# Kernel tuning notes

Hardware: AMD Instinct MI355X
Metric: run time of the kernel (lower is better)

Reference implementation:

```python
import jax, jax.numpy as jnp
import numpy as np
from jax import lax

HS, WS = 8, 8  # pattern_size


def setup_inputs() -> dict:
    key = jax.random.key(0)
    k1, k2, k3 = jax.random.split(key, 3)
    B, C, T, H, W = 2, 64, 16, 112, 112
    Cout, K = 64, 3
    x = jax.random.normal(k1, (B, C, T, H, W), dtype=jnp.float32)
    # one independent Conv3d weight/bias per (h, w) phase in the 8x8 pattern
    weight = jax.random.normal(k2, (HS, WS, Cout, C, K, K, K), dtype=jnp.float32) * 0.05
    bias = jax.random.normal(k3, (HS, WS, Cout), dtype=jnp.float32) * 0.05
    return {"x": x, "weight": weight, "bias": bias}


def reference(x, weight, bias):
    hs, ws = HS, WS
    B, C, T, H, W = x.shape
    Cout = weight.shape[2]
    # torch F.pad(x, (hs-1, hs-1, ws-1, ws-1, 1, 1)): W padded by hs-1, H by ws-1, T by 1
    paded = jnp.pad(x, ((0, 0), (0, 0), (1, 1), (ws - 1, ws - 1), (hs - 1, hs - 1)))
    Ho, Wo = H // hs, W // ws  # conv output spatial size per phase: (H-3)//8 + 1 = H//8
    rows = []
    for h in range(hs):
        cols = []
        for w in range(ws):
            sl = paded[:, :, :, h:H + h, w:W + w]  # [B, C, T+2, H, W]
            y = lax.conv_general_dilated(
                sl, weight[h, w],
                window_strides=(1, hs, ws), padding='VALID',
                dimension_numbers=('NCDHW', 'OIDHW', 'NCDHW'))  # [B, Cout, T, Ho, Wo]
            cols.append(y + bias[h, w][None, :, None, None, None])
        rows.append(jnp.stack(cols, 0))
    res = jnp.stack(rows, 0)  # [hs, ws, B, Cout, T, Ho, Wo]
    # out[:, :, :, h + hs*i, w + ws*j] = res[h, w, :, :, :, i, j]
    out = jnp.transpose(res, (2, 3, 4, 5, 0, 6, 1))  # [B, Cout, T, Ho, hs, Wo, ws]
    return out.reshape(B, Cout, T, H, W)
```

## Files before the change

kernel.cpp:

```cpp
#include <hip/hip_runtime.h>
#include <hip/hip_bf16.h>
#include <stdint.h>

typedef __attribute__((ext_vector_type(8))) short short8;
typedef __attribute__((ext_vector_type(4))) float f32x4;

#define XPP_BYTES 66355200ull
#define XPP_SLACK 65536ull
#define WPP_BYTES 14155776ull

__device__ __forceinline__ void gl2lds16(const void* g, void* l) {
    __builtin_amdgcn_global_load_lds(
        (const __attribute__((address_space(1))) unsigned int*)g,
        (__attribute__((address_space(3))) unsigned int*)l, 16, 0, 0);
}

__global__ __launch_bounds__(256)
void bzero(uint4* __restrict__ xpp) {
    const uint4 z = {0u, 0u, 0u, 0u};
    const int total = 935936;
    for (int idx = blockIdx.x * 256 + threadIdx.x; idx < total;
         idx += gridDim.x * 256) {
        int u;
        if (idx < 276480) {
            int slab = idx / 2160, off = idx % 2160;
            u = slab * 32400 + off;
        } else if (idx < 534528) {
            int k = idx - 276480;
            int run = k / 144, off = k % 144;
            int slab = run / 14, rho = run % 14 + 1;
            u = slab * 32400 + rho * 2160 + off;
        } else {
            int k = idx - 534528;
            int run = k / 8, off = k % 8;
            int slab = run / 392, r2 = run % 392;
            int rho = r2 / 28 + 1, r3 = r2 % 28;
            int cwo = r3 / 2 + 1, d = (r3 & 1) * 17;
            u = slab * 32400 + rho * 2160 + cwo * 144 + d * 8 + off;
        }
        xpp[u] = z;
    }
}

__global__ __launch_bounds__(512)
void xform_x(const float* __restrict__ xin, __hip_bfloat16* __restrict__ xpp) {
    extern __shared__ __hip_bfloat16 Xl[];
    const int bid = blockIdx.x;
    const int rho = bid % 14, d = (bid / 14) % 16, b = bid / 224;
    const int tid = threadIdx.x;
    for (int f = tid; f < 64 * 8 * 28; f += 512) {
        int ci = f / 224, rem = f % 224;
        int r = rem / 28, c4 = (rem % 28) * 4;
        const float4 v = *(const float4*)&xin[
            ((((size_t)b * 64 + ci) * 16 + d) * 112 + (rho * 8 + r)) * 112 + c4];
        const float vv[4] = {v.x, v.y, v.z, v.w};
#pragma unroll
        for (int u = 0; u < 4; ++u) {
            int c = c4 + u;
            Xl[(r * 112 + c) * 64 + (ci ^ ((c & 7) << 3))] = __float2bfloat16(vv[u]);
        }
    }
    __syncthreads();
    for (int f = tid; f < 896 * 8; f += 512) {
        int pos = f >> 3, j = f & 7;
        int r = pos / 112, c = pos % 112;
        int cw = c & 7, cwo = c >> 3;
        uint4 v = *(const uint4*)&Xl[pos * 64 + ((j * 8) ^ ((c & 7) << 3))];
        size_t dst = (((((size_t)(r * 8 + cw) * 2 + b) * 15 + (rho + 1)) * 15
                       + (cwo + 1)) * 18 + (d + 1)) * 64 + j * 8;
        *(uint4*)(xpp + dst) = v;
    }
}

__global__ __launch_bounds__(256)
void xform_w(const float* __restrict__ wt, __hip_bfloat16* __restrict__ wpp) {
    __shared__ __hip_bfloat16 lw[8 * 27 * 72];
    const int hw = blockIdx.x >> 3, cc = blockIdx.x & 7;
    for (int f = threadIdx.x; f < 8 * 64 * 27; f += 256) {
        int k = f % 27, ci = (f / 27) % 64, co = f / (27 * 64);
        float v = wt[(size_t)hw * 110592 + (size_t)(cc * 8 + co) * 1728 + ci * 27 + k];
        lw[(co * 27 + k) * 72 + ci] = __float2bfloat16(v);
    }
    __syncthreads();
    for (int f = threadIdx.x; f < 27 * 8 * 8; f += 256) {
        int cic = f % 8, co = (f / 8) % 8, k = f / 64;
        uint4 v = *(const uint4*)&lw[(co * 27 + k) * 72 + cic * 8];
        size_t dst = (((size_t)hw * 27 + k) * 64 + (cc * 8 + co)) * 64 + cic * 8;
        *(uint4*)(wpp + dst) = v;
    }
}


#define STG(S) do {                                                          \
    const int s3_ = (S);                                                     \
    const int rr_ = s3_ >> 1, kh_ = rr_ / 3, kw_ = rr_ % 3;                  \
    const int r0_ = h + kh_ - 7, c0_ = w + kw_ - 7;                          \
    const char* ap_ = (const char*)xpp +                                     \
        (size_t)(((((r0_ & 7) * 8 + (c0_ & 7)) * 2 + b) * 15                 \
                  + ((r0_ >> 3) + 1 + mc)) * 15 + ((c0_ >> 3) + 1)) * 2304   \
        + (s3_ & 1) * 64;                                                    \
    char* Ad_ = smem + (s3_ & 3) * 16384;                                    \
    _Pragma("unroll")                                                        \
    for (int i_ = 0; i_ < 4; ++i_)                                           \
        gl2lds16(ap_ + srcoff[i_], Ad_ + (uint32_t)(tid + i_ * 256) * 16);   \
} while (0)

#define LDB(R, DST) do {                                                     \
    const char* bp_ = wbase + (size_t)(R) * 8192;                            \
    _Pragma("unroll")                                                        \
    for (int kd_ = 0; kd_ < 3; ++kd_)                                        \
    _Pragma("unroll")                                                        \
    for (int ks_ = 0; ks_ < 2; ++ks_)                                        \
    _Pragma("unroll")                                                        \
    for (int n_ = 0; n_ < 2; ++n_)                                           \
        DST[kd_ * 4 + ks_ * 2 + n_] = *(const short8*)(                      \
            bp_ + kd_ * 73728 + (ng * 2 + n_) * 2048 + ks_ * 64 + bofs);     \
} while (0)

#define WINDOW(S, R, CUR, NXT, KS, DOB, DOA, WAITN) do {                     \
    if ((WAITN) == 0)      asm volatile("s_waitcnt vmcnt(0)" ::: "memory");  \
    else if ((WAITN) == 4) asm volatile("s_waitcnt vmcnt(4)" ::: "memory");  \
    else if ((WAITN) == 8) asm volatile("s_waitcnt vmcnt(8)" ::: "memory");  \
    else                   asm volatile("s_waitcnt vmcnt(20)" ::: "memory"); \
    __builtin_amdgcn_s_barrier();                                            \
    {   const char* Ab_ = smem + ((S) & 3) * 16384;                          \
        _Pragma("unroll")                                                    \
        for (int kd = 0; kd < 3; ++kd) {                                     \
            short8 af_[7];                                                   \
            _Pragma("unroll")                                                \
            for (int j_ = 0; j_ < 7; ++j_)                                   \
                af_[j_] = *(const short8*)(Ab_ + (mg * 7 + j_) * 1152        \
                                           + rofs[kd]);                      \
            if (kd == 0) {                                                   \
                __builtin_amdgcn_sched_barrier(0);                           \
                if (DOB) LDB((R) + 1, NXT);                                  \
                if (DOA) STG((S) + 3);                                       \
                __builtin_amdgcn_sched_barrier(0);                           \
            }                                                                \
            __builtin_amdgcn_s_setprio(1);                                   \
            _Pragma("unroll")                                                \
            for (int j_ = 0; j_ < 7; ++j_)                                   \
                _Pragma("unroll")                                            \
                for (int n_ = 0; n_ < 2; ++n_)                               \
                    acc[j_][n_] = __builtin_amdgcn_mfma_f32_16x16x32_bf16(   \
                        af_[j_], CUR[kd * 4 + (KS) * 2 + n_],                \
                        acc[j_][n_], 0, 0, 0);                               \
            __builtin_amdgcn_s_setprio(0);                                   \
        } }                                                                  \
} while (0)

__global__ __launch_bounds__(256, 2)
void patgemm(const __hip_bfloat16* __restrict__ xpp,
             const __hip_bfloat16* __restrict__ wpp,
             const float* __restrict__ bs,
             float* __restrict__ out) {
    extern __shared__ char smem[];
    const int bid = blockIdx.x;
    const int h = bid & 7, k = bid >> 3;
    const int w = k & 7, b = (k >> 3) & 1, mc = k >> 4;
    const int hw = h * 8 + w;
    const int tid = threadIdx.x, wv = tid >> 6, lane = tid & 63;
    const int col = lane & 15, quad = lane >> 4;
    const int mg = wv >> 1, ng = wv & 1;

    uint32_t srcoff[4];
#pragma unroll
    for (int i = 0; i < 4; ++i) {
        int u = tid + i * 256; if (u > 1007) u = 1007;
        int wo = u / 72, rem = u % 72;
        int d = rem >> 2, qp = rem & 3, q = qp ^ ((d >> 1) & 3);
        srcoff[i] = (uint32_t)(wo * 2304 + d * 128 + q * 16);
    }
    uint32_t rofs[3];
#pragma unroll
    for (int kd = 0; kd < 3; ++kd)
        rofs[kd] = (uint32_t)((col + kd) * 64
            + ((quad ^ (((col + kd) >> 1) & 3)) << 4));
    const uint32_t bofs = (uint32_t)(col * 128 + quad * 16);

    f32x4 acc[7][2];
#pragma unroll
    for (int j = 0; j < 7; ++j)
#pragma unroll
        for (int n = 0; n < 2; ++n) acc[j][n] = (f32x4){0.f, 0.f, 0.f, 0.f};

    const char* wbase = (const char*)wpp + (size_t)hw * 27 * 8192;
    short8 bfrA[12], bfrB[12];

    STG(0);
    __builtin_amdgcn_sched_barrier(0);
    LDB(0, bfrA);
    __builtin_amdgcn_sched_barrier(0);
    STG(1);
    STG(2);

#pragma unroll 1
    for (int rp = 0; rp < 4; ++rp) {
        const int ra = 2 * rp, rb = 2 * rp + 1;
        WINDOW(2 * ra,     ra, bfrA, bfrB, 0, 1, 1, 8);
        WINDOW(2 * ra + 1, ra, bfrA, bfrB, 1, 0, 1, 20);
        WINDOW(2 * rb,     rb, bfrB, bfrA, 0, 1, 1, 8);
        WINDOW(2 * rb + 1, rb, bfrB, bfrA, 1, 0, (rb < 7), 20);
    }
    WINDOW(16, 8, bfrA, bfrB, 0, 0, 0, 4);
    WINDOW(17, 8, bfrA, bfrB, 1, 0, 0, 0);

    const float* bsl = bs + hw * 64;
    const int y = 8 * mc + h;
#pragma unroll
    for (int j = 0; j < 7; ++j) {
        const int wo = mg * 7 + j;
        const int x = 8 * wo + w;
#pragma unroll
        for (int n = 0; n < 2; ++n) {
            const int co = (ng * 2 + n) * 16 + col;
            const float bv = bsl[co];
#pragma unroll
            for (int jj = 0; jj < 4; ++jj) {
                const int t = quad * 4 + jj;
                out[((((size_t)b * 64 + co) * 16 + t) * 112 + y) * 112 + x]
                    = acc[j][n][jj] + bv;
            }
        }
    }
}

#define XL_ROWSTRIDE 116
#define WL_WSTRIDE (17*27)

__global__ __launch_bounds__(256, 3)
void patconv3d_fp32(const float* __restrict__ xin,
                    const float* __restrict__ wt,
                    const float* __restrict__ bs,
                    float* __restrict__ out) {
    __shared__ float Xl[3*3*7*XL_ROWSTRIDE];
    __shared__ float Wl[8*WL_WSTRIDE];
    const int bid = blockIdx.x;
    const int ct = bid & 3, hb = (bid >> 2) & 1, h = (bid >> 3) & 7;
    const int t = (bid >> 6) & 15, b = (bid >> 10) & 1;
    const int tid = threadIdx.x;
    const int xl = tid & 127, cg = tid >> 7;
    const int xr = (xl < 112) ? xl : 111;
    const int wq = xl & 7;
    float acc[8][7];
#pragma unroll
    for (int c = 0; c < 8; ++c)
#pragma unroll
        for (int ho = 0; ho < 7; ++ho) acc[c][ho] = 0.f;
    for (int ci = 0; ci < 64; ++ci) {
        __syncthreads();
        for (int idx = tid; idx < 3 * 3 * 7 * 114; idx += 256) {
            int c = idx % 114, rest = idx / 114;
            int ho = rest % 7; rest /= 7;
            int kh = rest % 3, kd = rest / 3;
            int r = 8 * (hb * 7 + ho) + h + kh - 7;
            int d = t + kd - 1, colx = c - 7;
            float v = 0.f;
            if (r >= 0 && d >= 0 && d < 16 && colx >= 0)
                v = xin[(((size_t)(b * 64 + ci) * 16 + d) * 112 + r) * 112 + colx];
            Xl[((kd * 3 + kh) * 7 + ho) * XL_ROWSTRIDE + c] = v;
        }
        for (int idx = tid; idx < 8 * 16 * 27; idx += 256) {
            int k2 = idx % 27, rest = idx / 27;
            int co_l = rest % 16, wi = rest / 16;
            Wl[wi * WL_WSTRIDE + co_l * 27 + k2] =
                wt[(((size_t)(h * 8 + wi) * 64 + (ct * 16 + co_l)) * 64 + ci) * 27 + k2];
        }
        __syncthreads();
#pragma unroll
        for (int kd = 0; kd < 3; ++kd)
#pragma unroll
            for (int kh = 0; kh < 3; ++kh)
#pragma unroll
                for (int kw = 0; kw < 3; ++kw) {
                    const int k2 = (kd * 3 + kh) * 3 + kw;
                    float xv[7];
#pragma unroll
                    for (int ho = 0; ho < 7; ++ho)
                        xv[ho] = Xl[((kd * 3 + kh) * 7 + ho) * XL_ROWSTRIDE + xr + kw];
                    float wv[8];
#pragma unroll
                    for (int c = 0; c < 8; ++c)
                        wv[c] = Wl[wq * WL_WSTRIDE + (cg * 8 + c) * 27 + k2];
#pragma unroll
                    for (int c = 0; c < 8; ++c)
#pragma unroll
                        for (int ho = 0; ho < 7; ++ho)
                            acc[c][ho] += wv[c] * xv[ho];
                }
    }
    if (xl < 112) {
#pragma unroll
        for (int c = 0; c < 8; ++c) {
            const int co = ct * 16 + cg * 8 + c;
            const float bv = bs[(h * 8 + wq) * 64 + co];
#pragma unroll
            for (int ho = 0; ho < 7; ++ho) {
                const int y = 8 * (hb * 7 + ho) + h;
                out[(((size_t)(b * 64 + co) * 16 + t) * 112 + y) * 112 + xl] = acc[c][ho] + bv;
            }
        }
    }
}

extern "C" void kernel_launch(void* const* d_in, const int* in_sizes, int n_in,
                              void* d_out, int out_size, void* d_ws, size_t ws_size,
                              hipStream_t stream) {
    const float* x  = (const float*)d_in[0];
    const float* wg = (const float*)d_in[1];
    const float* bi = (const float*)d_in[2];
    float* out = (float*)d_out;
    if (ws_size >= XPP_BYTES + XPP_SLACK + WPP_BYTES) {
        __hip_bfloat16* xpp = (__hip_bfloat16*)d_ws;
        __hip_bfloat16* wpp = (__hip_bfloat16*)((char*)d_ws + XPP_BYTES + XPP_SLACK);
        bzero<<<1024, 256, 0, stream>>>((uint4*)d_ws);
        xform_x<<<448, 512, 114688, stream>>>(x, xpp);
        xform_w<<<512, 256, 0, stream>>>(wg, wpp);
        patgemm<<<1792, 256, 65536, stream>>>(xpp, wpp, bi, out);
    } else {
        patconv3d_fp32<<<2048, 256, 0, stream>>>(x, wg, bi, out);
    }
}
```

Before: 303.0 us.

## Double patgemm waves per block, splitting N across four waves

The patgemm block grows from 256 to 512 threads. Each wave now owns one 16-wide slice of output channels instead of two, which halves the per-wave B fragments and accumulators. Weight fragments are prefetched one K-step (stage) ahead instead of one filter row ahead, and the wait counts and LDS staging loads are rebalanced across the larger block. The aim is to cut register pressure, raise occupancy and latency hiding, and shorten each wave's serial MFMA chain. The cost is that each A fragment read from LDS is reused by fewer MFMAs, so LDS traffic per FLOP roughly doubles, and each stage needs more barriers.

```diff
diff --git a/kernel.cpp b/kernel.cpp
--- a/kernel.cpp
+++ b/kernel.cpp
@@ -101,27 +101,22 @@
         + (s3_ & 1) * 64;                                                    \
     char* Ad_ = smem + (s3_ & 3) * 16384;                                    \
     _Pragma("unroll")                                                        \
-    for (int i_ = 0; i_ < 4; ++i_)                                           \
-        gl2lds16(ap_ + srcoff[i_], Ad_ + (uint32_t)(tid + i_ * 256) * 16);   \
+    for (int i_ = 0; i_ < 2; ++i_)                                           \
+        gl2lds16(ap_ + srcoff[i_], Ad_ + (uint32_t)(tid + i_ * 512) * 16);   \
 } while (0)
 
-#define LDB(R, DST) do {                                                     \
-    const char* bp_ = wbase + (size_t)(R) * 8192;                            \
+#define LDB(S, DST) do {                                                     \
+    const int sb_ = (S);                                                     \
+    const char* bp_ = wbase + (size_t)(sb_ >> 1) * 8192 + (sb_ & 1) * 64;    \
     _Pragma("unroll")                                                        \
     for (int kd_ = 0; kd_ < 3; ++kd_)                                        \
-    _Pragma("unroll")                                                        \
-    for (int ks_ = 0; ks_ < 2; ++ks_)                                        \
-    _Pragma("unroll")                                                        \
-    for (int n_ = 0; n_ < 2; ++n_)                                           \
-        DST[kd_ * 4 + ks_ * 2 + n_] = *(const short8*)(                      \
-            bp_ + kd_ * 73728 + (ng * 2 + n_) * 2048 + ks_ * 64 + bofs);     \
+        DST[kd_] = *(const short8*)(bp_ + kd_ * 73728 + ng * 2048 + bofs);   \
 } while (0)
 
-#define WINDOW(S, R, CUR, NXT, KS, DOB, DOA, WAITN) do {                     \
+#define WINDOW(S, CUR, NXT, DOB, DOA, WAITN) do {                            \
     if ((WAITN) == 0)      asm volatile("s_waitcnt vmcnt(0)" ::: "memory");  \
     else if ((WAITN) == 4) asm volatile("s_waitcnt vmcnt(4)" ::: "memory");  \
-    else if ((WAITN) == 8) asm volatile("s_waitcnt vmcnt(8)" ::: "memory");  \
-    else                   asm volatile("s_waitcnt vmcnt(20)" ::: "memory"); \
+    else                   asm volatile("s_waitcnt vmcnt(2)" ::: "memory");  \
     __builtin_amdgcn_s_barrier();                                            \
     {   const char* Ab_ = smem + ((S) & 3) * 16384;                          \
         _Pragma("unroll")                                                    \
@@ -133,23 +128,21 @@
                                            + rofs[kd]);                      \
             if (kd == 0) {                                                   \
                 __builtin_amdgcn_sched_barrier(0);                           \
-                if (DOB) LDB((R) + 1, NXT);                                  \
+                if (DOB) LDB((S) + 1, NXT);                                  \
+                __builtin_amdgcn_sched_barrier(0);                           \
                 if (DOA) STG((S) + 3);                                       \
                 __builtin_amdgcn_sched_barrier(0);                           \
             }                                                                \
             __builtin_amdgcn_s_setprio(1);                                   \
             _Pragma("unroll")                                                \
             for (int j_ = 0; j_ < 7; ++j_)                                   \
-                _Pragma("unroll")                                            \
-                for (int n_ = 0; n_ < 2; ++n_)                               \
-                    acc[j_][n_] = __builtin_amdgcn_mfma_f32_16x16x32_bf16(   \
-                        af_[j_], CUR[kd * 4 + (KS) * 2 + n_],                \
-                        acc[j_][n_], 0, 0, 0);                               \
+                acc[j_] = __builtin_amdgcn_mfma_f32_16x16x32_bf16(           \
+                    af_[j_], CUR[kd], acc[j_], 0, 0, 0);                     \
             __builtin_amdgcn_s_setprio(0);                                   \
         } }                                                                  \
 } while (0)
 
-__global__ __launch_bounds__(256, 2)
+__global__ __launch_bounds__(512, 4)
 void patgemm(const __hip_bfloat16* __restrict__ xpp,
              const __hip_bfloat16* __restrict__ wpp,
              const float* __restrict__ bs,
@@ -161,12 +154,12 @@
     const int hw = h * 8 + w;
     const int tid = threadIdx.x, wv = tid >> 6, lane = tid & 63;
     const int col = lane & 15, quad = lane >> 4;
-    const int mg = wv >> 1, ng = wv & 1;
-
-    uint32_t srcoff[4];
-#pragma unroll
-    for (int i = 0; i < 4; ++i) {
-        int u = tid + i * 256; if (u > 1007) u = 1007;
+    const int mg = wv >> 2, ng = wv & 3;
+
+    uint32_t srcoff[2];
+#pragma unroll
+    for (int i = 0; i < 2; ++i) {
+        int u = tid + i * 512; if (u > 1007) u = 1007;
         int wo = u / 72, rem = u % 72;
         int d = rem >> 2, qp = rem & 3, q = qp ^ ((d >> 1) & 3);
         srcoff[i] = (uint32_t)(wo * 2304 + d * 128 + q * 16);
@@ -178,14 +171,12 @@
             + ((quad ^ (((col + kd) >> 1) & 3)) << 4));
     const uint32_t bofs = (uint32_t)(col * 128 + quad * 16);
 
-    f32x4 acc[7][2];
-#pragma unroll
-    for (int j = 0; j < 7; ++j)
-#pragma unroll
-        for (int n = 0; n < 2; ++n) acc[j][n] = (f32x4){0.f, 0.f, 0.f, 0.f};
+    f32x4 acc[7];
+#pragma unroll
+    for (int j = 0; j < 7; ++j) acc[j] = (f32x4){0.f, 0.f, 0.f, 0.f};
 
     const char* wbase = (const char*)wpp + (size_t)hw * 27 * 8192;
-    short8 bfrA[12], bfrB[12];
+    short8 bfrA[3], bfrB[3];
 
     STG(0);
     __builtin_amdgcn_sched_barrier(0);
@@ -194,33 +185,30 @@
     STG(1);
     STG(2);
 
+    WINDOW(0, bfrA, bfrB, 1, 1, 4);
 #pragma unroll 1
-    for (int rp = 0; rp < 4; ++rp) {
-        const int ra = 2 * rp, rb = 2 * rp + 1;
-        WINDOW(2 * ra,     ra, bfrA, bfrB, 0, 1, 1, 8);
-        WINDOW(2 * ra + 1, ra, bfrA, bfrB, 1, 0, 1, 20);
-        WINDOW(2 * rb,     rb, bfrB, bfrA, 0, 1, 1, 8);
-        WINDOW(2 * rb + 1, rb, bfrB, bfrA, 1, 0, (rb < 7), 20);
-    }
-    WINDOW(16, 8, bfrA, bfrB, 0, 0, 0, 4);
-    WINDOW(17, 8, bfrA, bfrB, 1, 0, 0, 0);
+    for (int kp = 0; kp < 7; ++kp) {
+        const int s1 = 2 * kp + 1;
+        WINDOW(s1,     bfrB, bfrA, 1, 1, 2);
+        WINDOW(s1 + 1, bfrA, bfrB, 1, 1, 2);
+    }
+    WINDOW(15, bfrB, bfrA, 1, 0, 2);
+    WINDOW(16, bfrA, bfrB, 1, 0, 0);
+    WINDOW(17, bfrB, bfrA, 0, 0, 0);
 
     const float* bsl = bs + hw * 64;
     const int y = 8 * mc + h;
+    const int co = ng * 16 + col;
+    const float bv = bsl[co];
 #pragma unroll
     for (int j = 0; j < 7; ++j) {
         const int wo = mg * 7 + j;
         const int x = 8 * wo + w;
 #pragma unroll
-        for (int n = 0; n < 2; ++n) {
-            const int co = (ng * 2 + n) * 16 + col;
-            const float bv = bsl[co];
-#pragma unroll
-            for (int jj = 0; jj < 4; ++jj) {
-                const int t = quad * 4 + jj;
-                out[((((size_t)b * 64 + co) * 16 + t) * 112 + y) * 112 + x]
-                    = acc[j][n][jj] + bv;
-            }
+        for (int jj = 0; jj < 4; ++jj) {
+            const int t = quad * 4 + jj;
+            out[((((size_t)b * 64 + co) * 16 + t) * 112 + y) * 112 + x]
+                = acc[j][jj] + bv;
         }
     }
 }
@@ -316,7 +304,7 @@
         bzero<<<1024, 256, 0, stream>>>((uint4*)d_ws);
         xform_x<<<448, 512, 114688, stream>>>(x, xpp);
         xform_w<<<512, 256, 0, stream>>>(wg, wpp);
-        patgemm<<<1792, 256, 65536, stream>>>(xpp, wpp, bi, out);
+        patgemm<<<1792, 512, 65536, stream>>>(xpp, wpp, bi, out);
     } else {
         patconv3d_fp32<<<2048, 256, 0, stream>>>(x, wg, bi, out);
     }
```

Measured after the change: 298.0 us. Within noise of the previous version (-1.6%).

## Switch patgemm to 32x32x16 MFMA with 7-wave blocks covering two output rows

Applied to the files above, without the earlier changes.

Rewrites the main GEMM kernel to use 32x32x16 bf16 MFMA tiles instead of 16x16x32. Each 448-thread block now covers two output rows (mcp) with 7 waves, which halves the grid. The weight layout is repacked so each lane loads its B fragment with a contiguous 16-byte read. The A-tile staging moves to a 3-stage ring of larger LDS buffers, and the K loop is fully unrolled with per-window prefetch. Occupancy drops to one block per CU with more LDS per block, in exchange for higher MFMA efficiency and more reuse of each weight load.

```diff
diff --git a/kernel.cpp b/kernel.cpp
--- a/kernel.cpp
+++ b/kernel.cpp
@@ -3,7 +3,7 @@
 #include <stdint.h>
 
 typedef __attribute__((ext_vector_type(8))) short short8;
-typedef __attribute__((ext_vector_type(4))) float f32x4;
+typedef __attribute__((ext_vector_type(16))) float f32x16;
 
 #define XPP_BYTES 66355200ull
 #define XPP_SLACK 65536ull
@@ -73,7 +73,7 @@
 }
 
 __global__ __launch_bounds__(256)
-void xform_w(const float* __restrict__ wt, __hip_bfloat16* __restrict__ wpp) {
+void xform_w(const float* __restrict__ wt, uint4* __restrict__ wpp) {
     __shared__ __hip_bfloat16 lw[8 * 27 * 72];
     const int hw = blockIdx.x >> 3, cc = blockIdx.x & 7;
     for (int f = threadIdx.x; f < 8 * 64 * 27; f += 256) {
@@ -83,143 +83,151 @@
     }
     __syncthreads();
     for (int f = threadIdx.x; f < 27 * 8 * 8; f += 256) {
-        int cic = f % 8, co = (f / 8) % 8, k = f / 64;
-        uint4 v = *(const uint4*)&lw[(co * 27 + k) * 72 + cic * 8];
-        size_t dst = (((size_t)hw * 27 + k) * 64 + (cc * 8 + co)) * 64 + cic * 8;
-        *(uint4*)(wpp + dst) = v;
-    }
-}
-
-
-#define STG(S) do {                                                          \
-    const int s3_ = (S);                                                     \
-    const int rr_ = s3_ >> 1, kh_ = rr_ / 3, kw_ = rr_ % 3;                  \
-    const int r0_ = h + kh_ - 7, c0_ = w + kw_ - 7;                          \
+        int cic = f % 8, co8 = (f / 8) % 8, k = f / 64;
+        uint4 v = *(const uint4*)&lw[(co8 * 27 + k) * 72 + cic * 8];
+        const int co = cc * 8 + co8;
+        size_t dst = ((size_t)hw * 27 + k) * 512 + (cic >> 1) * 128
+                   + (co >> 5) * 64 + (cic & 1) * 32 + (co & 31);
+        wpp[dst] = v;
+    }
+}
+
+
+#define WAITVM_(N) asm volatile("s_waitcnt vmcnt(" #N ")" ::: "memory")
+#define WAITVM(N) WAITVM_(N)
+
+#define STG(S) do { if ((S) < 18) {                                          \
+    const int rr_ = (S) >> 1, hf_ = (S) & 1;                                 \
+    const int r0_ = h + (rr_ / 3) - 7, c0_ = w + (rr_ % 3) - 7;              \
     const char* ap_ = (const char*)xpp +                                     \
         (size_t)(((((r0_ & 7) * 8 + (c0_ & 7)) * 2 + b) * 15                 \
-                  + ((r0_ >> 3) + 1 + mc)) * 15 + ((c0_ >> 3) + 1)) * 2304   \
-        + (s3_ & 1) * 64;                                                    \
-    char* Ad_ = smem + (s3_ & 3) * 16384;                                    \
+                  + ((r0_ >> 3) + 1 + 2 * mcp)) * 15 + ((c0_ >> 3) + 1))     \
+        * 2304 + hf_ * 64;                                                   \
+    char* Ad_ = smem + ((S) % 3) * 35840;                                    \
     _Pragma("unroll")                                                        \
-    for (int i_ = 0; i_ < 4; ++i_)                                           \
-        gl2lds16(ap_ + srcoff[i_], Ad_ + (uint32_t)(tid + i_ * 256) * 16);   \
-} while (0)
-
-#define LDB(R, DST) do {                                                     \
-    const char* bp_ = wbase + (size_t)(R) * 8192;                            \
+    for (int i_ = 0; i_ < 5; ++i_)                                           \
+        gl2lds16(ap_ + srcoff[i_], Ad_ + (uint32_t)(tid + i_ * 448) * 16);   \
+} } while (0)
+
+#define LDB(S, DST) do { if ((S) < 18) {                                     \
+    const int rr_ = (S) >> 1, hf_ = (S) & 1;                                 \
     _Pragma("unroll")                                                        \
     for (int kd_ = 0; kd_ < 3; ++kd_)                                        \
     _Pragma("unroll")                                                        \
     for (int ks_ = 0; ks_ < 2; ++ks_)                                        \
     _Pragma("unroll")                                                        \
     for (int n_ = 0; n_ < 2; ++n_)                                           \
-        DST[kd_ * 4 + ks_ * 2 + n_] = *(const short8*)(                      \
-            bp_ + kd_ * 73728 + (ng * 2 + n_) * 2048 + ks_ * 64 + bofs);     \
-} while (0)
-
-#define WINDOW(S, R, CUR, NXT, KS, DOB, DOA, WAITN) do {                     \
-    if ((WAITN) == 0)      asm volatile("s_waitcnt vmcnt(0)" ::: "memory");  \
-    else if ((WAITN) == 4) asm volatile("s_waitcnt vmcnt(4)" ::: "memory");  \
-    else if ((WAITN) == 8) asm volatile("s_waitcnt vmcnt(8)" ::: "memory");  \
-    else                   asm volatile("s_waitcnt vmcnt(20)" ::: "memory"); \
+        DST[kd_ * 4 + ks_ * 2 + n_] = *(const short8*)(wbase                 \
+            + (size_t)((kd_ * 9 + rr_) * 4 + hf_ * 2 + ks_) * 2048          \
+            + n_ * 1024 + (uint32_t)lane * 16);                              \
+} } while (0)
+
+#define WIN(S, CUR, NXT, WN) do {                                            \
+    WAITVM(WN);                                                              \
     __builtin_amdgcn_s_barrier();                                            \
-    {   const char* Ab_ = smem + ((S) & 3) * 16384;                          \
+    LDB((S) + 1, NXT);                                                       \
+    __builtin_amdgcn_sched_barrier(0);                                       \
+    STG((S) + 2);                                                            \
+    __builtin_amdgcn_sched_barrier(0);                                       \
+    {   const char* Ab_ = smem + ((S) % 3) * 35840;                          \
         _Pragma("unroll")                                                    \
-        for (int kd = 0; kd < 3; ++kd) {                                     \
-            short8 af_[7];                                                   \
-            _Pragma("unroll")                                                \
-            for (int j_ = 0; j_ < 7; ++j_)                                   \
-                af_[j_] = *(const short8*)(Ab_ + (mg * 7 + j_) * 1152        \
-                                           + rofs[kd]);                      \
-            if (kd == 0) {                                                   \
-                __builtin_amdgcn_sched_barrier(0);                           \
-                if (DOB) LDB((R) + 1, NXT);                                  \
-                if (DOA) STG((S) + 3);                                       \
-                __builtin_amdgcn_sched_barrier(0);                           \
-            }                                                                \
+        for (int kd = 0; kd < 3; ++kd)                                       \
+        _Pragma("unroll")                                                    \
+        for (int ks = 0; ks < 2; ++ks) {                                     \
+            short8 a0_ = *(const short8*)(Ab_ + woB + rofs[kd][ks]);         \
+            short8 a1_ = *(const short8*)(Ab_ + 16128 + woB + rofs[kd][ks]); \
             __builtin_amdgcn_s_setprio(1);                                   \
-            _Pragma("unroll")                                                \
-            for (int j_ = 0; j_ < 7; ++j_)                                   \
-                _Pragma("unroll")                                            \
-                for (int n_ = 0; n_ < 2; ++n_)                               \
-                    acc[j_][n_] = __builtin_amdgcn_mfma_f32_16x16x32_bf16(   \
-                        af_[j_], CUR[kd * 4 + (KS) * 2 + n_],                \
-                        acc[j_][n_], 0, 0, 0);                               \
+            acc00 = __builtin_amdgcn_mfma_f32_32x32x16_bf16(                 \
+                a0_, CUR[kd * 4 + ks * 2 + 0], acc00, 0, 0, 0);              \
+            acc01 = __builtin_amdgcn_mfma_f32_32x32x16_bf16(                 \
+                a0_, CUR[kd * 4 + ks * 2 + 1], acc01, 0, 0, 0);              \
+            acc10 = __builtin_amdgcn_mfma_f32_32x32x16_bf16(                 \
+                a1_, CUR[kd * 4 + ks * 2 + 0], acc10, 0, 0, 0);              \
+            acc11 = __builtin_amdgcn_mfma_f32_32x32x16_bf16(                 \
+                a1_, CUR[kd * 4 + ks * 2 + 1], acc11, 0, 0, 0);              \
             __builtin_amdgcn_s_setprio(0);                                   \
         } }                                                                  \
 } while (0)
 
-__global__ __launch_bounds__(256, 2)
+__global__ __launch_bounds__(448, 1)
 void patgemm(const __hip_bfloat16* __restrict__ xpp,
-             const __hip_bfloat16* __restrict__ wpp,
+             const char* __restrict__ wpp,
              const float* __restrict__ bs,
              float* __restrict__ out) {
     extern __shared__ char smem[];
     const int bid = blockIdx.x;
     const int h = bid & 7, k = bid >> 3;
-    const int w = k & 7, b = (k >> 3) & 1, mc = k >> 4;
+    const int w = k & 7, b = (k >> 3) & 1, mcp = k >> 4;
     const int hw = h * 8 + w;
     const int tid = threadIdx.x, wv = tid >> 6, lane = tid & 63;
-    const int col = lane & 15, quad = lane >> 4;
-    const int mg = wv >> 1, ng = wv & 1;
-
-    uint32_t srcoff[4];
-#pragma unroll
-    for (int i = 0; i < 4; ++i) {
-        int u = tid + i * 256; if (u > 1007) u = 1007;
-        int wo = u / 72, rem = u % 72;
-        int d = rem >> 2, qp = rem & 3, q = qp ^ ((d >> 1) & 3);
-        srcoff[i] = (uint32_t)(wo * 2304 + d * 128 + q * 16);
-    }
-    uint32_t rofs[3];
+    const int c31 = lane & 31, hi = lane >> 5;
+
+    uint32_t srcoff[5];
+#pragma unroll
+    for (int i = 0; i < 5; ++i) {
+        int u = tid + i * 448; if (u > 2015) u = 2015;
+        int rs = u / 1008, rem = u - rs * 1008;
+        int wo = rem / 72, r2 = rem - wo * 72;
+        int d = r2 >> 2, gp = r2 & 3, g = gp ^ ((d >> 1) & 3);
+        srcoff[i] = (uint32_t)(rs * 34560 + wo * 2304 + d * 128 + g * 16);
+    }
+    const uint32_t woB = (uint32_t)((2 * wv + ((lane >> 4) & 1)) * 1152);
+    uint32_t rofs[3][2];
 #pragma unroll
     for (int kd = 0; kd < 3; ++kd)
-        rofs[kd] = (uint32_t)((col + kd) * 64
-            + ((quad ^ (((col + kd) >> 1) & 3)) << 4));
-    const uint32_t bofs = (uint32_t)(col * 128 + quad * 16);
-
-    f32x4 acc[7][2];
-#pragma unroll
-    for (int j = 0; j < 7; ++j)
-#pragma unroll
-        for (int n = 0; n < 2; ++n) acc[j][n] = (f32x4){0.f, 0.f, 0.f, 0.f};
-
-    const char* wbase = (const char*)wpp + (size_t)hw * 27 * 8192;
-    short8 bfrA[12], bfrB[12];
-
+#pragma unroll
+        for (int ks = 0; ks < 2; ++ks) {
+            int d = (lane & 15) + kd;
+            rofs[kd][ks] = (uint32_t)(d * 64
+                + (((ks * 2 + hi) ^ ((d >> 1) & 3)) << 4));
+        }
+
+    f32x16 acc00 = {0}, acc01 = {0}, acc10 = {0}, acc11 = {0};
+
+    const char* wbase = wpp + (size_t)hw * 27 * 8192;
+    short8 bfr0[12], bfr1[12];
+
+    LDB(0, bfr0);
+    __builtin_amdgcn_sched_barrier(0);
     STG(0);
-    __builtin_amdgcn_sched_barrier(0);
-    LDB(0, bfrA);
-    __builtin_amdgcn_sched_barrier(0);
     STG(1);
-    STG(2);
-
-#pragma unroll 1
-    for (int rp = 0; rp < 4; ++rp) {
-        const int ra = 2 * rp, rb = 2 * rp + 1;
-        WINDOW(2 * ra,     ra, bfrA, bfrB, 0, 1, 1, 8);
-        WINDOW(2 * ra + 1, ra, bfrA, bfrB, 1, 0, 1, 20);
-        WINDOW(2 * rb,     rb, bfrB, bfrA, 0, 1, 1, 8);
-        WINDOW(2 * rb + 1, rb, bfrB, bfrA, 1, 0, (rb < 7), 20);
-    }
-    WINDOW(16, 8, bfrA, bfrB, 0, 0, 0, 4);
-    WINDOW(17, 8, bfrA, bfrB, 1, 0, 0, 0);
+
+    WIN(0,  bfr0, bfr1, 5);
+    WIN(1,  bfr1, bfr0, 17);
+    WIN(2,  bfr0, bfr1, 17);
+    WIN(3,  bfr1, bfr0, 17);
+    WIN(4,  bfr0, bfr1, 17);
+    WIN(5,  bfr1, bfr0, 17);
+    WIN(6,  bfr0, bfr1, 17);
+    WIN(7,  bfr1, bfr0, 17);
+    WIN(8,  bfr0, bfr1, 17);
+    WIN(9,  bfr1, bfr0, 17);
+    WIN(10, bfr0, bfr1, 17);
+    WIN(11, bfr1, bfr0, 17);
+    WIN(12, bfr0, bfr1, 17);
+    WIN(13, bfr1, bfr0, 17);
+    WIN(14, bfr0, bfr1, 17);
+    WIN(15, bfr1, bfr0, 17);
+    WIN(16, bfr0, bfr1, 17);
+    WIN(17, bfr1, bfr0, 12);
 
     const float* bsl = bs + hw * 64;
-    const int y = 8 * mc + h;
-#pragma unroll
-    for (int j = 0; j < 7; ++j) {
-        const int wo = mg * 7 + j;
-        const int x = 8 * wo + w;
+#pragma unroll
+    for (int mi = 0; mi < 2; ++mi) {
+        const int y = 8 * (2 * mcp + mi) + h;
 #pragma unroll
         for (int n = 0; n < 2; ++n) {
-            const int co = (ng * 2 + n) * 16 + col;
+            const f32x16 A = (mi == 0) ? (n == 0 ? acc00 : acc01)
+                                       : (n == 0 ? acc10 : acc11);
+            const int co = n * 32 + c31;
             const float bv = bsl[co];
 #pragma unroll
-            for (int jj = 0; jj < 4; ++jj) {
-                const int t = quad * 4 + jj;
-                out[((((size_t)b * 64 + co) * 16 + t) * 112 + y) * 112 + x]
-                    = acc[j][n][jj] + bv;
+            for (int r = 0; r < 16; ++r) {
+                const int row = (r & 3) + 8 * (r >> 2) + 4 * hi;
+                const int wo = 2 * wv + (row >> 4);
+                const int t = row & 15;
+                out[(((size_t)(b * 64 + co) * 16 + t) * 112 + y) * 112
+                    + 8 * wo + w] = A[r] + bv;
             }
         }
     }
@@ -312,11 +320,11 @@
     float* out = (float*)d_out;
     if (ws_size >= XPP_BYTES + XPP_SLACK + WPP_BYTES) {
         __hip_bfloat16* xpp = (__hip_bfloat16*)d_ws;
-        __hip_bfloat16* wpp = (__hip_bfloat16*)((char*)d_ws + XPP_BYTES + XPP_SLACK);
+        char* wpp = (char*)d_ws + XPP_BYTES + XPP_SLACK;
         bzero<<<1024, 256, 0, stream>>>((uint4*)d_ws);
         xform_x<<<448, 512, 114688, stream>>>(x, xpp);
-        xform_w<<<512, 256, 0, stream>>>(wg, wpp);
-        patgemm<<<1792, 256, 65536, stream>>>(xpp, wpp, bi, out);
+        xform_w<<<512, 256, 0, stream>>>(wg, (uint4*)wpp);
+        patgemm<<<896, 448, 107520, stream>>>(xpp, wpp, bi, out);
     } else {
         patconv3d_fp32<<<2048, 256, 0, stream>>>(x, wg, bi, out);
     }
```

Result: slower. 309.4 us (+2.1%).
